# Kernel tuning notes

Measured on AMD Instinct MI355X. Metric: run time of the kernel, lower is better.

Reference implementation:

```python
import jax, jax.numpy as jnp
import numpy as np
import math

L, E, NH, P, MLP_H, OUT = 4, 512, 8, 16, 2048, 1024
HD = E // NH
EPS = 1e-6

def layernorm(x, g, b):
    mu = jnp.mean(x, axis=-1, keepdims=True)
    var = jnp.mean(jnp.square(x - mu), axis=-1, keepdims=True)
    return g * (x - mu) / jnp.sqrt(var + EPS) + b

def gelu_tanh(x):
    c = jnp.float32(0.7978845608028654)
    return 0.5 * x * (1.0 + jnp.tanh(c * (x + 0.044715 * x * x * x)))

def sinusoidal_pos(T, dim):
    pos = jnp.arange(T, dtype=jnp.float32)[:, None]
    div = jnp.exp(jnp.arange(0, dim, 2, dtype=jnp.float32) * (-math.log(10000.0) / dim))
    pe = jnp.concatenate([jnp.sin(pos * div), jnp.cos(pos * div)], axis=1)
    return pe[:, :dim]  # [T, dim] (all sins then all cos, matching source)

def _heads(y, B, T):
    return jnp.transpose(y.reshape(B, T, NH, HD), (0, 2, 1, 3))  # [B,H,T,D]

def self_attn(x, Wqkv, Wo):
    B, T, _ = x.shape
    q, k, v = jnp.split(x @ Wqkv, 3, axis=-1)
    q, k, v = _heads(q, B, T), _heads(k, B, T), _heads(v, B, T)
    logits = jnp.einsum('bhqd,bhkd->bhqk', q, k) * (HD ** -0.5)
    attn = jax.nn.softmax(logits, axis=-1)
    out = jnp.einsum('bhqk,bhkd->bhqd', attn, v)
    out = jnp.transpose(out, (0, 2, 1, 3)).reshape(B, T, E)
    return out @ Wo

def cross_attn(xq, xkv, Wq, Wkv, Wo):
    B, Tq, _ = xq.shape
    Tk = xkv.shape[1]
    q = _heads(xq @ Wq, B, Tq)
    k, v = jnp.split(xkv @ Wkv, 2, axis=-1)
    k, v = _heads(k, B, Tk), _heads(v, B, Tk)
    logits = jnp.einsum('bhqd,bhkd->bhqk', q, k) * (HD ** -0.5)
    attn = jax.nn.softmax(logits, axis=-1)
    out = jnp.einsum('bhqk,bhkd->bhqd', attn, v)
    out = jnp.transpose(out, (0, 2, 1, 3)).reshape(B, Tq, E)
    return out @ Wo

def block(x, i, ln1_g, ln1_b, Wqkv, Wo, ln2_g, ln2_b, W1, b1, W2, b2):
    x = x + self_attn(layernorm(x, ln1_g[i], ln1_b[i]), Wqkv[i], Wo[i])
    h = layernorm(x, ln2_g[i], ln2_b[i])
    h = gelu_tanh(h @ W1[i] + b1[i]) @ W2[i] + b2[i]
    return x + h

def setup_inputs():
    key = jax.random.key(0)
    ks = jax.random.split(key, 16)
    B, HW = 8, 512
    w = lambda k, sh: jax.random.normal(k, sh, dtype=jnp.float32) * 0.02
    return {
        'img1': jax.random.normal(ks[0], (B, HW, HW, 3), dtype=jnp.float32),
        'img2': jax.random.normal(ks[1], (B, HW, HW, 3), dtype=jnp.float32),
        'patch_W': w(ks[2], (P, P, 3, E)),
        'cls_token': w(ks[3], (1, 1, E)),
        'cls_pos': w(ks[4], (1, 1, E)),
        'ln1_g': jnp.ones((L, E)), 'ln1_b': jnp.zeros((L, E)),
        'Wqkv': w(ks[5], (L, E, 3 * E)),
        'Wo': w(ks[6], (L, E, E)),
        'ln2_g': jnp.ones((L, E)), 'ln2_b': jnp.zeros((L, E)),
        'W1': w(ks[7], (L, E, MLP_H)), 'b1': jnp.zeros((L, MLP_H)),
        'W2': w(ks[8], (L, MLP_H, E)), 'b2': jnp.zeros((L, E)),
        'Wq_c': w(ks[9], (E, E)),
        'Wkv_c': w(ks[10], (E, 2 * E)),
        'Wo_c': w(ks[11], (E, E)),
        'nf_g': jnp.ones((E,)), 'nf_b': jnp.zeros((E,)),
        'Wdec': w(ks[12], (E, OUT)), 'bdec': jnp.zeros((OUT,)),
    }

def reference(img1, img2, patch_W, cls_token, cls_pos, ln1_g, ln1_b, Wqkv, Wo,
              ln2_g, ln2_b, W1, b1, W2, b2, Wq_c, Wkv_c, Wo_c, nf_g, nf_b, Wdec, bdec):
    B = img1.shape[0]
    def embed(img):
        p = jax.lax.conv_general_dilated(img, patch_W, (P, P), 'SAME',
                                         dimension_numbers=('NHWC', 'HWIO', 'NHWC'))
        Bh, Hh, Wh, C = p.shape
        t = p.reshape(Bh, Hh * Wh, C)
        return t + sinusoidal_pos(Hh * Wh, C)[None]
    t1, t2 = embed(img1), embed(img2)
    cls = jnp.tile(cls_token + cls_pos, (B, 1, 1))
    x1 = jnp.concatenate([cls, t1], axis=1)
    x2 = jnp.concatenate([cls, t2], axis=1)
    for i in range(L):
        x1 = block(x1, i, ln1_g, ln1_b, Wqkv, Wo, ln2_g, ln2_b, W1, b1, W2, b2)
        x2 = block(x2, i, ln1_g, ln1_b, Wqkv, Wo, ln2_g, ln2_b, W1, b1, W2, b2)
    cls1, tok1 = x1[:, :1, :], x1[:, 1:, :]
    cls2, tok2 = x2[:, :1, :], x2[:, 1:, :]
    cls1 = cls1 + cross_attn(cls1, tok2, Wq_c, Wkv_c, Wo_c)
    cls2 = cls2 + cross_attn(cls2, tok1, Wq_c, Wkv_c, Wo_c)
    cls_avg = 0.5 * (cls1[:, 0, :] + cls2[:, 0, :])
    cls_avg = layernorm(cls_avg, nf_g, nf_b)
    y = cls_avg @ Wdec + bdec
    return y[:, None, None, :]  # [B,1,1,1024]
```

## Files before the change

kernel.cpp:

```cpp
#include <hip/hip_runtime.h>
#include <stdint.h>
#include <math.h>

typedef __attribute__((ext_vector_type(4))) float f4;
typedef __attribute__((ext_vector_type(8))) __bf16 bf8;
typedef __attribute__((ext_vector_type(8))) short s8;
typedef __attribute__((ext_vector_type(4))) uint32_t u32x4;

#define DI __device__ __forceinline__

DI short f2bf(float f){
  union { float f; uint32_t u; } v; v.f = f;
  uint32_t r = v.u + 0x7fffu + ((v.u >> 16) & 1u);
  return (short)(r >> 16);
}
DI float bf2f(short s){
  union { uint32_t u; float f; } v; v.u = ((uint32_t)(uint16_t)s) << 16;
  return v.f;
}
DI uint32_t cvtpk(float lo, float hi){
  uint32_t r;
  asm("v_cvt_pk_bf16_f32 %0, %1, %2" : "=v"(r) : "v"(lo), "v"(hi));
  return r;
}
DI float fexp2(float x){
  float r;
  asm("v_exp_f32 %0, %1" : "=v"(r) : "v"(x));
  return r;
}
DI float gelu_f(float u){
  float zl = 2.3022081383f * u * fmaf(0.044715f, u*u, 1.f);
  return u * __builtin_amdgcn_rcpf(1.f + fexp2(-zl));
}
DI void gload16(const void* g, void* l){
  __builtin_amdgcn_global_load_lds((const __attribute__((address_space(1))) unsigned*)g,
                                   (__attribute__((address_space(3))) unsigned*)l, 16, 0, 0);
}

__global__ __launch_bounds__(256)
void k_transpose(const float* __restrict__ in, short* __restrict__ out, int K, int N, size_t stride)
{
  __shared__ float t[32][33];
  in  += (size_t)blockIdx.z * stride;
  out += (size_t)blockIdx.z * stride;
  int n0 = blockIdx.x*32, k0 = blockIdx.y*32;
  int tx = threadIdx.x, ty = threadIdx.y;
  #pragma unroll
  for (int i=0;i<32;i+=8) t[ty+i][tx] = in[(size_t)(k0+ty+i)*N + n0+tx];
  __syncthreads();
  #pragma unroll
  for (int i=0;i<32;i+=8) out[(size_t)(n0+ty+i)*K + k0+tx] = f2bf(t[tx][ty+i]);
}

__global__ void k_pe(float* __restrict__ pe)
{
  int p = blockIdx.x;
  for (int d = threadIdx.x; d < 512; d += 256){
    int j = (d < 256) ? d : d - 256;
    float div = expf((float)(2*j) * (-9.210340371976184f/512.f));
    float a = (float)p * div;
    pe[(size_t)p*512 + d] = (d < 256) ? sinf(a) : cosf(a);
  }
}

__global__ __launch_bounds__(256)
void k_gather(const float* __restrict__ img1, const float* __restrict__ img2, short* __restrict__ patches)
{
  int row = blockIdx.x;
  int img = row >> 13;
  int b   = (row >> 10) & 7;
  int p   = row & 1023;
  int ph = p >> 5, pw = p & 31;
  const float* src = (img ? img2 : img1) + (size_t)b*512*512*3;
  short* dst = patches + (size_t)row*768;
  for (int k = threadIdx.x; k < 768; k += 256){
    int i = k / 48; int rem = k - i*48; int j = rem / 3; int c = rem - j*3;
    int yy = ph*16 + i, xx = pw*16 + j;
    dst[k] = f2bf(src[((size_t)yy*512 + xx)*3 + c]);
  }
}

__global__ void k_zeropad(float* __restrict__ x)
{
  int idx = blockIdx.x; int ib = idx / 31; int t = 1025 + (idx - ib*31);
  x[((size_t)ib*1056 + t)*512 + threadIdx.x] = 0.f;
}
__global__ void k_cls(const float* __restrict__ ct, const float* __restrict__ cp, float* __restrict__ x)
{
  int ib = blockIdx.x; int e = threadIdx.x;
  x[(size_t)ib*1056*512 + e] = ct[e] + cp[e];
}

__global__ __launch_bounds__(256)
void k_layernorm(const float* __restrict__ x, short* __restrict__ y,
                 const float* __restrict__ g, const float* __restrict__ b)
{
  int row = blockIdx.x*4 + (threadIdx.x>>6);
  int l = threadIdx.x & 63;
  const float* xr = x + (size_t)row*512 + l*8;
  f4 v0 = *(const f4*)xr;
  f4 v1 = *(const f4*)(xr+4);
  float s = v0[0]+v0[1]+v0[2]+v0[3]+v1[0]+v1[1]+v1[2]+v1[3];
  float q = v0[0]*v0[0]+v0[1]*v0[1]+v0[2]*v0[2]+v0[3]*v0[3]
          + v1[0]*v1[0]+v1[1]*v1[1]+v1[2]*v1[2]+v1[3]*v1[3];
  #pragma unroll
  for (int m=1;m<64;m<<=1){ s += __shfl_xor(s,m); q += __shfl_xor(q,m); }
  float mu = s * 0.001953125f;
  float var = q * 0.001953125f - mu*mu;
  float rstd = rsqrtf(var + 1e-6f);
  const float* gp = g + l*8;
  const float* bp = b + l*8;
  float ov[8];
  #pragma unroll
  for (int j=0;j<8;j++){
    float xv = (j<4) ? v0[j] : v1[j-4];
    ov[j] = gp[j]*(xv-mu)*rstd + bp[j];
  }
  u32x4 pk;
  #pragma unroll
  for (int j=0;j<4;j++) pk[j] = cvtpk(ov[2*j], ov[2*j+1]);
  *(u32x4*)(y + (size_t)row*512 + l*8) = pk;
}

struct EpiArgs { short* outb; float* outf; const float* bias; const float* pe; short* vT; };

template<int EPI>
__global__ __launch_bounds__(256)
void k_gemm(const short* __restrict__ A, const short* __restrict__ Bt,
            int M, int N, int K, int gridX, EpiArgs ea)
{
  __shared__ short Al[128*64];
  __shared__ short Bl[128*64];
  const int tid = threadIdx.x;
  const int l = tid & 63;
  const int w = tid >> 6;
  const int wr = (w >> 1) * 64, wc = (w & 1) * 64;
  const int lr = l & 15, lg = l >> 4;
  const int nwg = gridDim.x;
  const int q8 = nwg >> 3;
  const int nb = (blockIdx.x & 7) * q8 + (blockIdx.x >> 3);
  const int brow = (nb / gridX) * 128, bcol = (nb % gridX) * 128;
  const short* Ab = A  + (size_t)brow * K;
  const short* Bb = Bt + (size_t)bcol * K;
  f4 acc[4][4];
  #pragma unroll
  for (int m=0;m<4;m++)
    #pragma unroll
    for (int n=0;n<4;n++){ acc[m][n][0]=0.f; acc[m][n][1]=0.f; acc[m][n][2]=0.f; acc[m][n][3]=0.f; }

  const int rsw = lr & 7;
  for (int kt = 0; kt < K; kt += 64){
    #pragma unroll
    for (int i=0;i<4;i++){
      int s   = i*256 + tid;
      int row = s >> 3;
      int gs  = (s & 7) ^ (row & 7);
      gload16(Ab + (size_t)row*K + kt + gs*8, &Al[s*8]);
      gload16(Bb + (size_t)row*K + kt + gs*8, &Bl[s*8]);
    }
    __syncthreads();
    #pragma unroll
    for (int ko=0;ko<2;ko++){
      bf8 af[4], bfr[4];
      const int ps = ((ko*4 + lg) ^ rsw) * 8;
      #pragma unroll
      for (int m=0;m<4;m++) af[m]  = *(const bf8*)&Al[(wr + m*16 + lr)*64 + ps];
      #pragma unroll
      for (int n=0;n<4;n++) bfr[n] = *(const bf8*)&Bl[(wc + n*16 + lr)*64 + ps];
      #pragma unroll
      for (int m=0;m<4;m++)
        #pragma unroll
        for (int n=0;n<4;n++)
          acc[m][n] = __builtin_amdgcn_mfma_f32_16x16x32_bf16(af[m], bfr[n], acc[m][n], 0, 0, 0);
    }
    __syncthreads();
  }

  #pragma unroll
  for (int m=0;m<4;m++){
    #pragma unroll
    for (int n=0;n<4;n++){
      const int row0 = brow + wr + m*16 + lg*4;
      const int col  = bcol + wc + n*16 + lr;
      float v0 = acc[m][n][0], v1 = acc[m][n][1], v2 = acc[m][n][2], v3 = acc[m][n][3];
      if (EPI == 0 || EPI == 1){
        if (EPI == 1 && col < 512){
          const float qs = 0.1803368801111204f;
          v0*=qs; v1*=qs; v2*=qs; v3*=qs;
        }
        uint32_t u01 = cvtpk(v0, v1), u23 = cvtpk(v2, v3);
        short s0 = (short)u01, s1 = (short)(u01>>16), s2 = (short)u23, s3 = (short)(u23>>16);
        ea.outb[(size_t)(row0+0)*N + col] = s0;
        ea.outb[(size_t)(row0+1)*N + col] = s1;
        ea.outb[(size_t)(row0+2)*N + col] = s2;
        ea.outb[(size_t)(row0+3)*N + col] = s3;
        if (EPI == 1 && col >= 1024){
          int ib = row0 / 1056, t = row0 - ib*1056;
          short* vtb = ea.vT + ((size_t)ib*512 + (col - 1024))*1056;
          vtb[t] = s0; vtb[t+1] = s1; vtb[t+2] = s2; vtb[t+3] = s3;
        }
      } else if (EPI == 2){
        float bv = ea.bias ? ea.bias[col] : 0.f;
        ea.outf[(size_t)(row0+0)*N + col] += v0 + bv;
        ea.outf[(size_t)(row0+1)*N + col] += v1 + bv;
        ea.outf[(size_t)(row0+2)*N + col] += v2 + bv;
        ea.outf[(size_t)(row0+3)*N + col] += v3 + bv;
      } else if (EPI == 5){
        float bv = ea.bias[col];
        float n0 = ea.outf[(size_t)(row0+0)*N + col] + v0 + bv;
        float n1 = ea.outf[(size_t)(row0+1)*N + col] + v1 + bv;
        float n2 = ea.outf[(size_t)(row0+2)*N + col] + v2 + bv;
        float n3 = ea.outf[(size_t)(row0+3)*N + col] + v3 + bv;
        ea.outf[(size_t)(row0+0)*N + col] = n0;
        ea.outf[(size_t)(row0+1)*N + col] = n1;
        ea.outf[(size_t)(row0+2)*N + col] = n2;
        ea.outf[(size_t)(row0+3)*N + col] = n3;
        uint32_t u01 = cvtpk(n0, n1), u23 = cvtpk(n2, n3);
        ea.outb[(size_t)(row0+0)*N + col] = (short)u01;
        ea.outb[(size_t)(row0+1)*N + col] = (short)(u01>>16);
        ea.outb[(size_t)(row0+2)*N + col] = (short)u23;
        ea.outb[(size_t)(row0+3)*N + col] = (short)(u23>>16);
      } else if (EPI == 3){
        float bv = ea.bias[col];
        float g0 = gelu_f(v0+bv), g1 = gelu_f(v1+bv), g2 = gelu_f(v2+bv), g3 = gelu_f(v3+bv);
        uint32_t u01 = cvtpk(g0, g1), u23 = cvtpk(g2, g3);
        ea.outb[(size_t)(row0+0)*N + col] = (short)u01;
        ea.outb[(size_t)(row0+1)*N + col] = (short)(u01>>16);
        ea.outb[(size_t)(row0+2)*N + col] = (short)u23;
        ea.outb[(size_t)(row0+3)*N + col] = (short)(u23>>16);
      } else if (EPI == 4){
        #pragma unroll
        for (int r=0;r<4;r++){
          int row = row0 + r;
          int ib = row >> 10, p = row & 1023;
          float v = (r==0)?v0:(r==1)?v1:(r==2)?v2:v3;
          ea.outf[((size_t)(ib*1056 + 1 + p))*512 + col] = v + ea.pe[(size_t)p*512 + col];
        }
      }
    }
  }
}

__global__ __launch_bounds__(256)
void k_attn(const short* __restrict__ qkv, const short* __restrict__ vT, short* __restrict__ aout)
{
  __shared__ __align__(16) short Kl[2][32*64];
  __shared__ __align__(16) short Vl[2][64*32];
  __shared__ short Pl[4][32*40];
  __shared__ float Sc[4][2][32];

  const int tid = threadIdx.x;
  const int w  = tid >> 6;
  const int nb = (blockIdx.x & 7) * (gridDim.x >> 3) + (blockIdx.x >> 3);
  const int u  = nb / 9;
  const int qtblk = nb - u*9;
  const int qtR = qtblk * 4 + w;
  const int qt  = qtR > 32 ? 32 : qtR;
  const int ib = u >> 3, h = u & 7;
  const int l = tid & 63, lr = l & 15, lg = l >> 4;
  const size_t rb = (size_t)ib * 1056;
  const int t0 = qt * 32;
  const float DEFER_THR = 11.541560327111707f;

  bf8 qf[2][2];
  #pragma unroll
  for (int nq=0;nq<2;nq++)
    #pragma unroll
    for (int ks=0;ks<2;ks++)
      qf[nq][ks] = *(const bf8*)&qkv[(rb + t0 + nq*16 + lr)*1536 + h*64 + ks*32 + lg*8];

  f4 o[2][4];
  float mrun[2], lrun[2];
  #pragma unroll
  for (int mq=0;mq<2;mq++)
    #pragma unroll
    for (int nd=0;nd<4;nd++){ o[mq][nd][0]=0.f; o[mq][nd][1]=0.f; o[mq][nd][2]=0.f; o[mq][nd][3]=0.f; }
  mrun[0]=mrun[1]=-1e30f; lrun[0]=lrun[1]=0.f;

  const int srow = tid >> 3;
  const short* kgp = &qkv[(rb + srow)*1536 + 512 + h*64 + (((tid & 7) ^ (srow & 7))*8)];
  const int vrow = tid >> 2;
  const short* vgp = &vT[((size_t)ib*512 + h*64 + vrow)*1056 + (((tid & 3) ^ (vrow & 3))*8)];
  auto STAGE = [&](int buf){
    gload16(kgp, &Kl[buf][tid*8]);
    gload16(vgp, &Vl[buf][tid*8]);
    kgp += 32*1536;
    vgp += 32;
  };

  int koff[2][2], voff[4];
  #pragma unroll
  for (int mk=0;mk<2;mk++)
    #pragma unroll
    for (int ks=0;ks<2;ks++)
      koff[mk][ks] = ((mk*16+lr)*8 + ((ks*4+lg) ^ (lr&7)))*8;
  #pragma unroll
  for (int nd=0;nd<4;nd++)
    voff[nd] = ((nd*16+lr)*4 + (lg ^ (lr&3)))*8;

  STAGE(0);

  for (int jt=0; jt<=32; jt++){
    const int cur = jt & 1;
    const bool MASK = (jt == 32);
    const int j0 = jt*32;
    __syncthreads();

    bf8 kc[2][2], vb[4];
    #pragma unroll
    for (int mk=0;mk<2;mk++)
      #pragma unroll
      for (int ks=0;ks<2;ks++)
        kc[mk][ks] = *(const bf8*)&Kl[cur][koff[mk][ks]];
    #pragma unroll
    for (int nd=0;nd<4;nd++)
      vb[nd] = *(const bf8*)&Vl[cur][voff[nd]];

    if (jt < 32) STAGE(cur^1);

    f4 st[2][2];
    #pragma unroll
    for (int mk=0;mk<2;mk++)
      #pragma unroll
      for (int nq=0;nq<2;nq++){ st[mk][nq][0]=0.f; st[mk][nq][1]=0.f; st[mk][nq][2]=0.f; st[mk][nq][3]=0.f; }
    __builtin_amdgcn_s_setprio(1);
    #pragma unroll
    for (int ks=0;ks<2;ks++)
      #pragma unroll
      for (int mk=0;mk<2;mk++)
        #pragma unroll
        for (int nq=0;nq<2;nq++)
          st[mk][nq] = __builtin_amdgcn_mfma_f32_16x16x32_bf16(kc[mk][ks], qf[nq][ks], st[mk][nq], 0, 0, 0);
    __builtin_amdgcn_s_setprio(0);

    float p8[2][8], mx[2];
    #pragma unroll
    for (int nq=0;nq<2;nq++){
      mx[nq] = -1e30f;
      #pragma unroll
      for (int mk=0;mk<2;mk++)
        #pragma unroll
        for (int r=0;r<4;r++){
          float v = st[mk][nq][r];
          if (MASK){
            int kk = j0 + mk*16 + lg*4 + r;
            v = (kk > 1024) ? -1e30f : v;
          }
          p8[nq][mk*4+r] = v;
          mx[nq] = fmaxf(mx[nq], v);
        }
      mx[nq] = fmaxf(mx[nq], __shfl_xor(mx[nq], 16));
      mx[nq] = fmaxf(mx[nq], __shfl_xor(mx[nq], 32));
    }

    bool ok = (mx[0] <= mrun[0] + DEFER_THR) && (mx[1] <= mrun[1] + DEFER_THR);
    if (__all(ok)){
      #pragma unroll
      for (int nq=0;nq<2;nq++){
        float rs = 0.f;
        #pragma unroll
        for (int i=0;i<8;i++){ float p = fexp2(p8[nq][i] - mrun[nq]); p8[nq][i] = p; rs += p; }
        rs += __shfl_xor(rs, 16);
        rs += __shfl_xor(rs, 32);
        lrun[nq] += rs;
        uint32_t* prow = (uint32_t*)&Pl[w][(nq*16 + lr)*40];
        #pragma unroll
        for (int mk=0;mk<2;mk++){
          prow[mk*8 + lg*2]     = cvtpk(p8[nq][mk*4+0], p8[nq][mk*4+1]);
          prow[mk*8 + lg*2 + 1] = cvtpk(p8[nq][mk*4+2], p8[nq][mk*4+3]);
        }
      }
      asm volatile("s_waitcnt lgkmcnt(0)" ::: "memory");
      __builtin_amdgcn_sched_barrier(0);
      bf8 pa[2];
      #pragma unroll
      for (int mq=0;mq<2;mq++) pa[mq] = *(const bf8*)&Pl[w][(mq*16 + lr)*40 + lg*8];
      __builtin_amdgcn_s_setprio(1);
      #pragma unroll
      for (int mq=0;mq<2;mq++)
        #pragma unroll
        for (int nd=0;nd<4;nd++)
          o[mq][nd] = __builtin_amdgcn_mfma_f32_16x16x32_bf16(pa[mq], vb[nd], o[mq][nd], 0, 0, 0);
      __builtin_amdgcn_s_setprio(0);
    } else {
      #pragma unroll
      for (int nq=0;nq<2;nq++){
        float mn = fmaxf(mrun[nq], mx[nq]);
        float sc = fexp2(mrun[nq] - mn);
        mrun[nq] = mn;
        float rs = 0.f;
        #pragma unroll
        for (int i=0;i<8;i++){ float p = fexp2(p8[nq][i] - mn); p8[nq][i] = p; rs += p; }
        rs += __shfl_xor(rs, 16);
        rs += __shfl_xor(rs, 32);
        lrun[nq] = lrun[nq]*sc + rs;
        Sc[w][0][nq*16 + lr] = sc;
        uint32_t* prow = (uint32_t*)&Pl[w][(nq*16 + lr)*40];
        #pragma unroll
        for (int mk=0;mk<2;mk++){
          prow[mk*8 + lg*2]     = cvtpk(p8[nq][mk*4+0], p8[nq][mk*4+1]);
          prow[mk*8 + lg*2 + 1] = cvtpk(p8[nq][mk*4+2], p8[nq][mk*4+3]);
        }
      }
      asm volatile("s_waitcnt lgkmcnt(0)" ::: "memory");
      __builtin_amdgcn_sched_barrier(0);
      f4 scv[2]; bf8 pa[2];
      #pragma unroll
      for (int mq=0;mq<2;mq++){
        scv[mq] = *(const f4*)&Sc[w][0][mq*16 + lg*4];
        pa[mq]  = *(const bf8*)&Pl[w][(mq*16 + lr)*40 + lg*8];
      }
      #pragma unroll
      for (int mq=0;mq<2;mq++)
        #pragma unroll
        for (int nd=0;nd<4;nd++){
          #pragma unroll
          for (int r=0;r<4;r++) o[mq][nd][r] *= scv[mq][r];
        }
      __builtin_amdgcn_s_setprio(1);
      #pragma unroll
      for (int mq=0;mq<2;mq++)
        #pragma unroll
        for (int nd=0;nd<4;nd++)
          o[mq][nd] = __builtin_amdgcn_mfma_f32_16x16x32_bf16(pa[mq], vb[nd], o[mq][nd], 0, 0, 0);
      __builtin_amdgcn_s_setprio(0);
    }
  }

  if (qtR <= 32){
    #pragma unroll
    for (int nq=0;nq<2;nq++) Sc[w][1][nq*16 + lr] = lrun[nq];
    asm volatile("s_waitcnt lgkmcnt(0)" ::: "memory");
    __builtin_amdgcn_sched_barrier(0);
    #pragma unroll
    for (int mq=0;mq<2;mq++){
      f4 lsv = *(const f4*)&Sc[w][1][mq*16 + lg*4];
      float i0 = __builtin_amdgcn_rcpf(lsv[0]);
      float i1 = __builtin_amdgcn_rcpf(lsv[1]);
      float i2 = __builtin_amdgcn_rcpf(lsv[2]);
      float i3 = __builtin_amdgcn_rcpf(lsv[3]);
      const size_t base = rb + t0 + mq*16 + lg*4;
      #pragma unroll
      for (int nd=0;nd<4;nd++){
        int col = h*64 + nd*16 + lr;
        uint32_t u01 = cvtpk(o[mq][nd][0]*i0, o[mq][nd][1]*i1);
        uint32_t u23 = cvtpk(o[mq][nd][2]*i2, o[mq][nd][3]*i3);
        aout[(base+0)*512 + col] = (short)u01;
        aout[(base+1)*512 + col] = (short)(u01>>16);
        aout[(base+2)*512 + col] = (short)u23;
        aout[(base+3)*512 + col] = (short)(u23>>16);
      }
    }
  }
}

__global__ __launch_bounds__(256)
void k_cross_q(const float* __restrict__ x, const float* __restrict__ Wq, float* __restrict__ qc)
{
  __shared__ float xs[512];
  int ib = blockIdx.x;
  const float* xr = x + (size_t)ib*1056*512;
  for (int e=threadIdx.x;e<512;e+=256) xs[e] = xr[e];
  __syncthreads();
  for (int n=threadIdx.x;n<512;n+=256){
    float acc = 0.f;
    for (int k=0;k<512;k++) acc += xs[k]*Wq[(size_t)k*512 + n];
    qc[(size_t)ib*512 + n] = acc;
  }
}

__global__ __launch_bounds__(64)
void k_cross_attn(const float* __restrict__ qc, const short* __restrict__ kv, float* __restrict__ oc)
{
  int u = blockIdx.x; int ib = u >> 3, h = u & 7;
  int img = ib >> 3, b = ib & 7;
  int sib = (1 - img)*8 + b;
  int l = threadIdx.x;
  __shared__ float qs[64];
  __shared__ float pl[1024];
  qs[l] = qc[(size_t)ib*512 + h*64 + l];
  __syncthreads();
  float lmax = -1e30f;
  for (int jj=0; jj<16; jj++){
    int j = jj*64 + l;
    const short* kr = kv + ((size_t)(sib*1056 + 1 + j))*1024 + h*64;
    float acc = 0.f;
    for (int d=0; d<64; d++) acc += qs[d]*bf2f(kr[d]);
    acc *= 0.125f;
    pl[j] = acc;
    lmax = fmaxf(lmax, acc);
  }
  #pragma unroll
  for (int m=1;m<64;m<<=1) lmax = fmaxf(lmax, __shfl_xor(lmax, m));
  __syncthreads();
  float lsum = 0.f;
  for (int jj=0; jj<16; jj++){
    int j = jj*64 + l;
    float p = __expf(pl[j] - lmax);
    pl[j] = p; lsum += p;
  }
  #pragma unroll
  for (int m=1;m<64;m<<=1) lsum += __shfl_xor(lsum, m);
  __syncthreads();
  float acc = 0.f;
  for (int j=0;j<1024;j++)
    acc += pl[j] * bf2f(kv[((size_t)(sib*1056 + 1 + j))*1024 + 512 + h*64 + l]);
  oc[(size_t)ib*512 + h*64 + l] = acc / lsum;
}

__global__ __launch_bounds__(256)
void k_cross_out(const float* __restrict__ x, const float* __restrict__ oc,
                 const float* __restrict__ Wo, float* __restrict__ cn)
{
  __shared__ float os[512];
  int ib = blockIdx.x;
  for (int e=threadIdx.x;e<512;e+=256) os[e] = oc[(size_t)ib*512+e];
  __syncthreads();
  for (int n=threadIdx.x;n<512;n+=256){
    float acc = 0.f;
    for (int k=0;k<512;k++) acc += os[k]*Wo[(size_t)k*512+n];
    cn[(size_t)ib*512+n] = x[(size_t)ib*1056*512 + n] + acc;
  }
}

__global__ __launch_bounds__(256)
void k_final(const float* __restrict__ cn, const float* __restrict__ nfg, const float* __restrict__ nfb,
             const float* __restrict__ Wdec, const float* __restrict__ bdec, float* __restrict__ out)
{
  int b = blockIdx.x >> 3;
  int n0 = (blockIdx.x & 7) * 128;
  __shared__ float an[512];
  __shared__ float red[8];
  int tid = threadIdx.x;
  float s = 0.f, q = 0.f;
  for (int e=tid;e<512;e+=256){
    float av = 0.5f*(cn[(size_t)b*512 + e] + cn[(size_t)(8+b)*512 + e]);
    an[e] = av; s += av; q += av*av;
  }
  #pragma unroll
  for (int m=1;m<64;m<<=1){ s += __shfl_xor(s,m); q += __shfl_xor(q,m); }
  int w = tid>>6;
  if ((tid&63)==0){ red[w] = s; red[4+w] = q; }
  __syncthreads();
  s = red[0]+red[1]+red[2]+red[3];
  q = red[4]+red[5]+red[6]+red[7];
  float mu = s*0.001953125f;
  float var = q*0.001953125f - mu*mu;
  float rstd = rsqrtf(var + 1e-6f);
  for (int e=tid;e<512;e+=256) an[e] = nfg[e]*(an[e]-mu)*rstd + nfb[e];
  __syncthreads();
  for (int n=tid;n<128;n+=256){
    int col = n0 + n;
    float acc = bdec[col];
    for (int e=0;e<512;e++) acc += an[e]*Wdec[(size_t)e*1024 + col];
    out[(size_t)b*1024 + col] = acc;
  }
}

extern "C" void kernel_launch(void* const* d_in, const int* in_sizes, int n_in,
                              void* d_out, int out_size, void* d_ws, size_t ws_size,
                              hipStream_t stream)
{
  (void)in_sizes; (void)n_in;
  const float* img1 = (const float*)d_in[0];
  const float* img2 = (const float*)d_in[1];
  const float* patchW = (const float*)d_in[2];
  const float* cls_t = (const float*)d_in[3];
  const float* cls_p = (const float*)d_in[4];
  const float* ln1g = (const float*)d_in[5];
  const float* ln1b = (const float*)d_in[6];
  const float* Wqkv = (const float*)d_in[7];
  const float* Wo   = (const float*)d_in[8];
  const float* ln2g = (const float*)d_in[9];
  const float* ln2b = (const float*)d_in[10];
  const float* W1   = (const float*)d_in[11];
  const float* b1   = (const float*)d_in[12];
  const float* W2   = (const float*)d_in[13];
  const float* b2   = (const float*)d_in[14];
  const float* Wqc  = (const float*)d_in[15];
  const float* Wkvc = (const float*)d_in[16];
  const float* Woc  = (const float*)d_in[17];
  const float* nfg  = (const float*)d_in[18];
  const float* nfb  = (const float*)d_in[19];
  const float* Wdec = (const float*)d_in[20];
  const float* bdec = (const float*)d_in[21];
  float* out = (float*)d_out;

  const size_t offA = 34603008, offB = 51904512, offC = 121110528, offD = 148111360;
  const size_t NEEDED = 148209664;
  if (ws_size < NEEDED){
    hipMemsetAsync(d_out, 0, (size_t)out_size*sizeof(float), stream);
    return;
  }
  char* ws = (char*)d_ws;
  float* x    = (float*)ws;
  short* y    = (short*)(ws + offA);
  short* attn = y;
  short* qkv  = (short*)(ws + offB);
  short* vT   = (short*)(ws + offB + 51904512);
  short* mh   = (short*)(ws + offB);
  short* patches = (short*)(ws + offB);
  float* pe   = (float*)(ws + offB + 25165824);
  short* kvc  = (short*)(ws + offB);
  short* wts  = (short*)(ws + offC);
  float* qc   = (float*)(ws + offD);
  float* oc   = (float*)(ws + offD + 32768);
  float* cn   = (float*)(ws + offD + 65536);

  short* patchWt = wts;
  short* WqkvT = wts + 393216;
  short* WoT   = wts + 3538944;
  short* W1T   = wts + 4587520;
  short* W2T   = wts + 8781824;
  short* WkvT  = wts + 12976128;

  dim3 tb(32,8,1);
  k_transpose<<<dim3(16,24,1), tb, 0, stream>>>(patchW, patchWt, 768, 512, (size_t)768*512);
  k_transpose<<<dim3(48,16,4), tb, 0, stream>>>(Wqkv, WqkvT, 512, 1536, (size_t)512*1536);
  k_transpose<<<dim3(16,16,4), tb, 0, stream>>>(Wo,   WoT,   512, 512,  (size_t)512*512);
  k_transpose<<<dim3(64,16,4), tb, 0, stream>>>(W1,   W1T,   512, 2048, (size_t)512*2048);
  k_transpose<<<dim3(16,64,4), tb, 0, stream>>>(W2,   W2T,   2048, 512, (size_t)2048*512);
  k_transpose<<<dim3(32,16,1), tb, 0, stream>>>(Wkvc, WkvT,  512, 1024, (size_t)512*1024);

  k_pe<<<1024, 256, 0, stream>>>(pe);
  k_gather<<<16384, 256, 0, stream>>>(img1, img2, patches);
  k_zeropad<<<496, 512, 0, stream>>>(x);
  k_cls<<<16, 512, 0, stream>>>(cls_t, cls_p, x);

  EpiArgs ea;
  ea = EpiArgs{nullptr, x, nullptr, pe, nullptr};
  k_gemm<4><<<512, 256, 0, stream>>>(patches, patchWt, 16384, 512, 768, 4, ea);

  for (int i=0;i<4;i++){
    k_layernorm<<<4224, 256, 0, stream>>>(x, y, ln1g + i*512, ln1b + i*512);
    ea = EpiArgs{qkv, nullptr, nullptr, nullptr, vT};
    k_gemm<1><<<1584, 256, 0, stream>>>(y, WqkvT + (size_t)i*1536*512, 16896, 1536, 512, 12, ea);
    k_attn<<<1152, 256, 0, stream>>>(qkv, vT, attn);
    ea = EpiArgs{nullptr, x, nullptr, nullptr, nullptr};
    k_gemm<2><<<528, 256, 0, stream>>>(attn, WoT + (size_t)i*512*512, 16896, 512, 512, 4, ea);
    k_layernorm<<<4224, 256, 0, stream>>>(x, y, ln2g + i*512, ln2b + i*512);
    ea = EpiArgs{mh, nullptr, b1 + i*2048, nullptr, nullptr};
    k_gemm<3><<<2112, 256, 0, stream>>>(y, W1T + (size_t)i*2048*512, 16896, 2048, 512, 16, ea);
    if (i == 3){
      ea = EpiArgs{y, x, b2 + i*512, nullptr, nullptr};
      k_gemm<5><<<528, 256, 0, stream>>>(mh, W2T + (size_t)i*512*2048, 16896, 512, 2048, 4, ea);
    } else {
      ea = EpiArgs{nullptr, x, b2 + i*512, nullptr, nullptr};
      k_gemm<2><<<528, 256, 0, stream>>>(mh, W2T + (size_t)i*512*2048, 16896, 512, 2048, 4, ea);
    }
  }

  ea = EpiArgs{kvc, nullptr, nullptr, nullptr, nullptr};
  k_gemm<0><<<1056, 256, 0, stream>>>(y, WkvT, 16896, 1024, 512, 8, ea);
  k_cross_q<<<16, 256, 0, stream>>>(x, Wqc, qc);
  k_cross_attn<<<128, 64, 0, stream>>>(qc, kvc, oc);
  k_cross_out<<<16, 256, 0, stream>>>(x, oc, Woc, cn);
  k_final<<<64, 256, 0, stream>>>(cn, nfg, nfb, Wdec, bdec, out);
}
```

Measured before the change: 1.524 ms.

## Add 256x256-tile GEMM kernel for QKV and MLP-up projections

Adds a 512-thread GEMM kernel with 256x256 output tiles (8 waves, each computing 128x64) and uses it for the QKV and W1 projections, which have wide N. Larger tiles raise arithmetic intensity and cut redundant global loads of A and B per output. The epilogue is factored into a shared helper. In exchange it uses 64KB LDS and 128 accumulator floats per lane, which lowers occupancy, and launches fewer workgroups (396/528), which risks a wave-quantization tail on 256 CUs. The XCD-aware block remap now also handles grid sizes that are not a multiple of 8.

```diff
diff --git a/kernel.cpp b/kernel.cpp
--- a/kernel.cpp
+++ b/kernel.cpp
@@ -123,6 +123,65 @@
 }
 
 struct EpiArgs { short* outb; float* outf; const float* bias; const float* pe; short* vT; };
+
+template<int EPI>
+DI void epilogue_frag(int row0, int col, int N, float v0, float v1, float v2, float v3, const EpiArgs& ea)
+{
+  if (EPI == 0 || EPI == 1){
+    if (EPI == 1 && col < 512){
+      const float qs = 0.1803368801111204f;
+      v0*=qs; v1*=qs; v2*=qs; v3*=qs;
+    }
+    uint32_t u01 = cvtpk(v0, v1), u23 = cvtpk(v2, v3);
+    short s0 = (short)u01, s1 = (short)(u01>>16), s2 = (short)u23, s3 = (short)(u23>>16);
+    ea.outb[(size_t)(row0+0)*N + col] = s0;
+    ea.outb[(size_t)(row0+1)*N + col] = s1;
+    ea.outb[(size_t)(row0+2)*N + col] = s2;
+    ea.outb[(size_t)(row0+3)*N + col] = s3;
+    if (EPI == 1 && col >= 1024){
+      int ib = row0 / 1056, t = row0 - ib*1056;
+      short* vtb = ea.vT + ((size_t)ib*512 + (col - 1024))*1056;
+      vtb[t] = s0; vtb[t+1] = s1; vtb[t+2] = s2; vtb[t+3] = s3;
+    }
+  } else if (EPI == 2){
+    float bv = ea.bias ? ea.bias[col] : 0.f;
+    ea.outf[(size_t)(row0+0)*N + col] += v0 + bv;
+    ea.outf[(size_t)(row0+1)*N + col] += v1 + bv;
+    ea.outf[(size_t)(row0+2)*N + col] += v2 + bv;
+    ea.outf[(size_t)(row0+3)*N + col] += v3 + bv;
+  } else if (EPI == 5){
+    float bv = ea.bias[col];
+    float n0 = ea.outf[(size_t)(row0+0)*N + col] + v0 + bv;
+    float n1 = ea.outf[(size_t)(row0+1)*N + col] + v1 + bv;
+    float n2 = ea.outf[(size_t)(row0+2)*N + col] + v2 + bv;
+    float n3 = ea.outf[(size_t)(row0+3)*N + col] + v3 + bv;
+    ea.outf[(size_t)(row0+0)*N + col] = n0;
+    ea.outf[(size_t)(row0+1)*N + col] = n1;
+    ea.outf[(size_t)(row0+2)*N + col] = n2;
+    ea.outf[(size_t)(row0+3)*N + col] = n3;
+    uint32_t u01 = cvtpk(n0, n1), u23 = cvtpk(n2, n3);
+    ea.outb[(size_t)(row0+0)*N + col] = (short)u01;
+    ea.outb[(size_t)(row0+1)*N + col] = (short)(u01>>16);
+    ea.outb[(size_t)(row0+2)*N + col] = (short)u23;
+    ea.outb[(size_t)(row0+3)*N + col] = (short)(u23>>16);
+  } else if (EPI == 3){
+    float bv = ea.bias[col];
+    float g0 = gelu_f(v0+bv), g1 = gelu_f(v1+bv), g2 = gelu_f(v2+bv), g3 = gelu_f(v3+bv);
+    uint32_t u01 = cvtpk(g0, g1), u23 = cvtpk(g2, g3);
+    ea.outb[(size_t)(row0+0)*N + col] = (short)u01;
+    ea.outb[(size_t)(row0+1)*N + col] = (short)(u01>>16);
+    ea.outb[(size_t)(row0+2)*N + col] = (short)u23;
+    ea.outb[(size_t)(row0+3)*N + col] = (short)(u23>>16);
+  } else if (EPI == 4){
+    float vv[4] = {v0,v1,v2,v3};
+    #pragma unroll
+    for (int r=0;r<4;r++){
+      int row = row0 + r;
+      int ib = row >> 10, p = row & 1023;
+      ea.outf[((size_t)(ib*1056 + 1 + p))*512 + col] = vv[r] + ea.pe[(size_t)p*512 + col];
+    }
+  }
+}
 
 template<int EPI>
 __global__ __launch_bounds__(256)
@@ -177,68 +236,72 @@
   }
 
   #pragma unroll
-  for (int m=0;m<4;m++){
-    #pragma unroll
-    for (int n=0;n<4;n++){
-      const int row0 = brow + wr + m*16 + lg*4;
-      const int col  = bcol + wc + n*16 + lr;
-      float v0 = acc[m][n][0], v1 = acc[m][n][1], v2 = acc[m][n][2], v3 = acc[m][n][3];
-      if (EPI == 0 || EPI == 1){
-        if (EPI == 1 && col < 512){
-          const float qs = 0.1803368801111204f;
-          v0*=qs; v1*=qs; v2*=qs; v3*=qs;
-        }
-        uint32_t u01 = cvtpk(v0, v1), u23 = cvtpk(v2, v3);
-        short s0 = (short)u01, s1 = (short)(u01>>16), s2 = (short)u23, s3 = (short)(u23>>16);
-        ea.outb[(size_t)(row0+0)*N + col] = s0;
-        ea.outb[(size_t)(row0+1)*N + col] = s1;
-        ea.outb[(size_t)(row0+2)*N + col] = s2;
-        ea.outb[(size_t)(row0+3)*N + col] = s3;
-        if (EPI == 1 && col >= 1024){
-          int ib = row0 / 1056, t = row0 - ib*1056;
-          short* vtb = ea.vT + ((size_t)ib*512 + (col - 1024))*1056;
-          vtb[t] = s0; vtb[t+1] = s1; vtb[t+2] = s2; vtb[t+3] = s3;
-        }
-      } else if (EPI == 2){
-        float bv = ea.bias ? ea.bias[col] : 0.f;
-        ea.outf[(size_t)(row0+0)*N + col] += v0 + bv;
-        ea.outf[(size_t)(row0+1)*N + col] += v1 + bv;
-        ea.outf[(size_t)(row0+2)*N + col] += v2 + bv;
-        ea.outf[(size_t)(row0+3)*N + col] += v3 + bv;
-      } else if (EPI == 5){
-        float bv = ea.bias[col];
-        float n0 = ea.outf[(size_t)(row0+0)*N + col] + v0 + bv;
-        float n1 = ea.outf[(size_t)(row0+1)*N + col] + v1 + bv;
-        float n2 = ea.outf[(size_t)(row0+2)*N + col] + v2 + bv;
-        float n3 = ea.outf[(size_t)(row0+3)*N + col] + v3 + bv;
-        ea.outf[(size_t)(row0+0)*N + col] = n0;
-        ea.outf[(size_t)(row0+1)*N + col] = n1;
-        ea.outf[(size_t)(row0+2)*N + col] = n2;
-        ea.outf[(size_t)(row0+3)*N + col] = n3;
-        uint32_t u01 = cvtpk(n0, n1), u23 = cvtpk(n2, n3);
-        ea.outb[(size_t)(row0+0)*N + col] = (short)u01;
-        ea.outb[(size_t)(row0+1)*N + col] = (short)(u01>>16);
-        ea.outb[(size_t)(row0+2)*N + col] = (short)u23;
-        ea.outb[(size_t)(row0+3)*N + col] = (short)(u23>>16);
-      } else if (EPI == 3){
-        float bv = ea.bias[col];
-        float g0 = gelu_f(v0+bv), g1 = gelu_f(v1+bv), g2 = gelu_f(v2+bv), g3 = gelu_f(v3+bv);
-        uint32_t u01 = cvtpk(g0, g1), u23 = cvtpk(g2, g3);
-        ea.outb[(size_t)(row0+0)*N + col] = (short)u01;
-        ea.outb[(size_t)(row0+1)*N + col] = (short)(u01>>16);
-        ea.outb[(size_t)(row0+2)*N + col] = (short)u23;
-        ea.outb[(size_t)(row0+3)*N + col] = (short)(u23>>16);
-      } else if (EPI == 4){
-        #pragma unroll
-        for (int r=0;r<4;r++){
-          int row = row0 + r;
-          int ib = row >> 10, p = row & 1023;
-          float v = (r==0)?v0:(r==1)?v1:(r==2)?v2:v3;
-          ea.outf[((size_t)(ib*1056 + 1 + p))*512 + col] = v + ea.pe[(size_t)p*512 + col];
-        }
-      }
-    }
-  }
+  for (int m=0;m<4;m++)
+    #pragma unroll
+    for (int n=0;n<4;n++)
+      epilogue_frag<EPI>(brow + wr + m*16 + lg*4, bcol + wc + n*16 + lr, N,
+                         acc[m][n][0], acc[m][n][1], acc[m][n][2], acc[m][n][3], ea);
+}
+
+template<int EPI>
+__global__ __launch_bounds__(512)
+void k_gemm256(const short* __restrict__ A, const short* __restrict__ Bt,
+               int M, int N, int K, int gridX, EpiArgs ea)
+{
+  __shared__ short Al[256*64];
+  __shared__ short Bl[256*64];
+  const int tid = threadIdx.x;
+  const int l = tid & 63;
+  const int w = tid >> 6;
+  const int wm = w >> 2, wn = w & 3;
+  const int lr = l & 15, lg = l >> 4;
+  const int nwg = gridDim.x;
+  const int q = nwg >> 3, r = nwg & 7;
+  const int xcd = blockIdx.x & 7, idx = blockIdx.x >> 3;
+  const int nb = (xcd < r ? xcd*(q+1) : r*(q+1) + (xcd - r)*q) + idx;
+  const int brow = (nb / gridX) * 256, bcol = (nb % gridX) * 256;
+  const short* Ab = A  + (size_t)brow * K;
+  const short* Bb = Bt + (size_t)bcol * K;
+  f4 acc[8][4];
+  #pragma unroll
+  for (int m=0;m<8;m++)
+    #pragma unroll
+    for (int n=0;n<4;n++){ acc[m][n][0]=0.f; acc[m][n][1]=0.f; acc[m][n][2]=0.f; acc[m][n][3]=0.f; }
+
+  const int rsw = lr & 7;
+  for (int kt = 0; kt < K; kt += 64){
+    #pragma unroll
+    for (int i=0;i<4;i++){
+      int s   = i*512 + tid;
+      int row = s >> 3;
+      int gs  = (s & 7) ^ (row & 7);
+      gload16(Ab + (size_t)row*K + kt + gs*8, &Al[s*8]);
+      gload16(Bb + (size_t)row*K + kt + gs*8, &Bl[s*8]);
+    }
+    __syncthreads();
+    #pragma unroll
+    for (int ko=0;ko<2;ko++){
+      const int ps = ((ko*4 + lg) ^ rsw) * 8;
+      bf8 af[8], bfr[4];
+      #pragma unroll
+      for (int m=0;m<8;m++) af[m]  = *(const bf8*)&Al[(wm*128 + m*16 + lr)*64 + ps];
+      #pragma unroll
+      for (int n=0;n<4;n++) bfr[n] = *(const bf8*)&Bl[(wn*64 + n*16 + lr)*64 + ps];
+      #pragma unroll
+      for (int m=0;m<8;m++)
+        #pragma unroll
+        for (int n=0;n<4;n++)
+          acc[m][n] = __builtin_amdgcn_mfma_f32_16x16x32_bf16(af[m], bfr[n], acc[m][n], 0, 0, 0);
+    }
+    __syncthreads();
+  }
+
+  #pragma unroll
+  for (int m=0;m<8;m++)
+    #pragma unroll
+    for (int n=0;n<4;n++)
+      epilogue_frag<EPI>(brow + wm*128 + m*16 + lg*4, bcol + wn*64 + n*16 + lr, N,
+                         acc[m][n][0], acc[m][n][1], acc[m][n][2], acc[m][n][3], ea);
 }
 
 __global__ __launch_bounds__(256)
@@ -634,13 +697,13 @@
   for (int i=0;i<4;i++){
     k_layernorm<<<4224, 256, 0, stream>>>(x, y, ln1g + i*512, ln1b + i*512);
     ea = EpiArgs{qkv, nullptr, nullptr, nullptr, vT};
-    k_gemm<1><<<1584, 256, 0, stream>>>(y, WqkvT + (size_t)i*1536*512, 16896, 1536, 512, 12, ea);
+    k_gemm256<1><<<396, 512, 0, stream>>>(y, WqkvT + (size_t)i*1536*512, 16896, 1536, 512, 6, ea);
     k_attn<<<1152, 256, 0, stream>>>(qkv, vT, attn);
     ea = EpiArgs{nullptr, x, nullptr, nullptr, nullptr};
     k_gemm<2><<<528, 256, 0, stream>>>(attn, WoT + (size_t)i*512*512, 16896, 512, 512, 4, ea);
     k_layernorm<<<4224, 256, 0, stream>>>(x, y, ln2g + i*512, ln2b + i*512);
     ea = EpiArgs{mh, nullptr, b1 + i*2048, nullptr, nullptr};
-    k_gemm<3><<<2112, 256, 0, stream>>>(y, W1T + (size_t)i*2048*512, 16896, 2048, 512, 16, ea);
+    k_gemm256<3><<<528, 512, 0, stream>>>(y, W1T + (size_t)i*2048*512, 16896, 2048, 512, 8, ea);
     if (i == 3){
       ea = EpiArgs{y, x, b2 + i*512, nullptr, nullptr};
       k_gemm<5><<<528, 256, 0, stream>>>(mh, W2T + (size_t)i*512*2048, 16896, 512, 2048, 4, ea);
```

After: 1.572 ms. 3.2% more time.
